# Kernel optimization log

Measured on AMD Instinct MI355X. Metric: run time of the kernel, lower is better.

Reference implementation:

```python
import jax, jax.numpy as jnp
import numpy as np

D_MODEL = 1024
NUM_HEADS = 16
D_K = D_MODEL // NUM_HEADS
BATCH = 4
SEQ = 2048


def setup_inputs() -> dict:
    key = jax.random.key(0)
    ks = jax.random.split(key, 12)
    s = 0.02
    inp = {
        "Q": jax.random.normal(ks[0], (BATCH, SEQ, D_MODEL), jnp.float32),
        "K": jax.random.normal(ks[1], (BATCH, SEQ, D_MODEL), jnp.float32),
        "V": jax.random.normal(ks[2], (BATCH, SEQ, D_MODEL), jnp.float32),
        "mask": jnp.tril(jnp.ones((SEQ, SEQ), jnp.int32)),  # causal: 0 = masked
        "Wq": jax.random.normal(ks[3], (D_MODEL, D_MODEL), jnp.float32) * s,
        "bq": jax.random.normal(ks[4], (D_MODEL,), jnp.float32) * s,
        "Wk": jax.random.normal(ks[5], (D_MODEL, D_MODEL), jnp.float32) * s,
        "bk": jax.random.normal(ks[6], (D_MODEL,), jnp.float32) * s,
        "Wv": jax.random.normal(ks[7], (D_MODEL, D_MODEL), jnp.float32) * s,
        "bv": jax.random.normal(ks[8], (D_MODEL,), jnp.float32) * s,
        "Wo": jax.random.normal(ks[9], (D_MODEL, D_MODEL), jnp.float32) * s,
        "bo": jax.random.normal(ks[10], (D_MODEL,), jnp.float32) * s,
    }
    return inp


def _split_heads(x):
    # (b, s, d_model) -> (b, h, s, d_k)
    b, s, _ = x.shape
    return x.reshape(b, s, NUM_HEADS, D_K).transpose(0, 2, 1, 3)


def reference(Q, K, V, mask, Wq, bq, Wk, bk, Wv, bv, Wo, bo):
    # Linear projections (torch Linear: x @ W^T + b)
    q = _split_heads(Q @ Wq.T + bq)  # (b, h, s, dk)
    k = _split_heads(K @ Wk.T + bk)
    v = _split_heads(V @ Wv.T + bv)
    scale = 1.0 / jnp.sqrt(jnp.asarray(D_K, q.dtype))
    scores = jnp.einsum("bhqd,bhkd->bhqk", q, k) * scale  # (b, h, s, s)
    scores = jnp.where(mask == 0, jnp.asarray(-jnp.inf, scores.dtype), scores)
    attn = jax.nn.softmax(scores, axis=-1)
    out = jnp.einsum("bhqk,bhkd->bhqd", attn, v)  # (b, h, s, dk)
    b, h, s, dk = out.shape
    out = out.transpose(0, 2, 1, 3).reshape(b, s, h * dk)  # combine heads
    return out @ Wo.T + bo
```

## Files before the change

kernel.cpp:

```cpp
#include <hip/hip_runtime.h>


typedef _Float16 f16;
typedef _Float16 f16x8 __attribute__((ext_vector_type(8)));
typedef _Float16 f16x4 __attribute__((ext_vector_type(4)));
typedef float floatx4 __attribute__((ext_vector_type(4)));

#define SEQ 2048
#define DM 1024
#define NH 16
#define DK 64
#define MR 8192

__device__ __forceinline__ void gl_lds16(const void* g, void* lds) {
    __builtin_amdgcn_global_load_lds(
        (const __attribute__((address_space(1))) unsigned int*)g,
        (__attribute__((address_space(3))) unsigned int*)lds,
        16, 0, 0);
}

struct ConvArgs {
    const float* s[7];
    f16* d[7];
};

__global__ __launch_bounds__(256) void convk(ConvArgs a) {
    int bx = blockIdx.x;
    int t, base;
    if (bx < 3 * 8192) { t = bx / 8192; base = bx - t * 8192; }
    else { int r = bx - 3 * 8192; t = 3 + r / 1024; base = r - (t - 3) * 1024; }
    int i = base * 256 + threadIdx.x;
    float4 v = ((const float4*)a.s[t])[i];
    f16x4 o;
    o.x = (f16)v.x; o.y = (f16)v.y; o.z = (f16)v.z; o.w = (f16)v.w;
    ((f16x4*)a.d[t])[i] = o;
}

template <int MODE>
__device__ __forceinline__ void gemm_body(
    const f16* __restrict__ A, const f16* __restrict__ W,
    const float* __restrict__ bias, void* __restrict__ outp,
    int m0, int n0, f16* As, f16* Bs)
{
    const int tid = threadIdx.x;
    const int wave = tid >> 6, lane = tid & 63;
    const int quad = lane >> 4, ln = lane & 15;
    const int wr = wave >> 1, wc = wave & 1;

    floatx4 acc[4][4] = {};

    for (int kt = 0; kt < 16; ++kt) {
        const int k0 = kt * 64;
#pragma unroll
        for (int s = 0; s < 4; ++s) {
            int c = s * 256 + tid;
            int row = c >> 3, lc = (c & 7) ^ (row & 7);
            gl_lds16(A + (size_t)(m0 + row) * 1024 + k0 + lc * 8,
                     (char*)As + (s * 256 + wave * 64) * 16);
        }
#pragma unroll
        for (int s = 0; s < 4; ++s) {
            int c = s * 256 + tid;
            int row = c >> 3, lc = (c & 7) ^ (row & 7);
            gl_lds16(W + (size_t)(n0 + row) * 1024 + k0 + lc * 8,
                     (char*)Bs + (s * 256 + wave * 64) * 16);
        }
        __syncthreads();
#pragma unroll
        for (int kk = 0; kk < 64; kk += 32) {
            const int cb = kk >> 3;
            f16x8 af[4], bf[4];
#pragma unroll
            for (int i = 0; i < 4; ++i) {
                int row = wr * 64 + i * 16 + ln;
                af[i] = *(const f16x8*)&As[row * 64 + (((cb + quad) ^ (ln & 7)) << 3)];
            }
#pragma unroll
            for (int j = 0; j < 4; ++j) {
                int row = wc * 64 + j * 16 + ln;
                bf[j] = *(const f16x8*)&Bs[row * 64 + (((cb + quad) ^ (ln & 7)) << 3)];
            }
#pragma unroll
            for (int i = 0; i < 4; ++i)
#pragma unroll
                for (int j = 0; j < 4; ++j)
                    acc[i][j] = __builtin_amdgcn_mfma_f32_16x16x32_f16(
                        af[i], bf[j], acc[i][j], 0, 0, 0);
        }
        __syncthreads();
    }

#pragma unroll
    for (int i = 0; i < 4; ++i) {
#pragma unroll
        for (int j = 0; j < 4; ++j) {
            int col = n0 + wc * 64 + j * 16 + ln;
            float bc = bias[col];
            int rowb = m0 + wr * 64 + i * 16 + quad * 4;
#pragma unroll
            for (int r = 0; r < 4; ++r) {
                float v = acc[i][j][r] + bc;
                int rm = rowb + r;
                if (MODE == 2) {
                    ((float*)outp)[(size_t)rm * 1024 + col] = v;
                } else {
                    int bb = rm >> 11, ss = rm & 2047;
                    int hh = col >> 6, dd = col & 63;
                    f16* o = (f16*)outp;
                    if (MODE == 0)
                        o[(((size_t)(bb * 16 + hh)) * 2048 + ss) * 64 + dd] = (f16)v;
                    else
                        o[(((size_t)(bb * 16 + hh)) * 64 + dd) * 2048 + ss] = (f16)v;
                }
            }
        }
    }
}

struct G3Args {
    const f16* A[3]; const f16* W[3]; const float* b[3]; f16* o[3];
};

__global__ __launch_bounds__(256, 4) void gemm_qkv(G3Args g) {
    __shared__ alignas(16) f16 As[128 * 64];
    __shared__ alignas(16) f16 Bs[128 * 64];
    const int z = blockIdx.z;
    const int m0 = blockIdx.x * 128, n0 = blockIdx.y * 128;
    if (z < 2)
        gemm_body<0>(g.A[z], g.W[z], g.b[z], g.o[z], m0, n0, As, Bs);
    else
        gemm_body<1>(g.A[2], g.W[2], g.b[2], g.o[2], m0, n0, As, Bs);
}

__global__ __launch_bounds__(256, 4) void gemm_out(
    const f16* __restrict__ A, const f16* __restrict__ W,
    const float* __restrict__ bias, float* __restrict__ outp)
{
    __shared__ alignas(16) f16 As[128 * 64];
    __shared__ alignas(16) f16 Bs[128 * 64];
    gemm_body<2>(A, W, bias, outp, blockIdx.x * 128, blockIdx.y * 128, As, Bs);
}

template <bool DIAG>
__device__ __forceinline__ void attn_iter(
    const f16* kb, const f16* vb, int k0, int q0,
    f16* ks, f16* vs, f16* pslot,
    int tid, int wave, int quad, int ln,
    const f16x8 (&aq)[2][2], const f16x8& ones,
    floatx4 (&oacc)[2][4], floatx4 (&lacc)[2])
{
#pragma unroll
    for (int s = 0; s < 4; ++s) {
        int c = s * 256 + tid;
        int row = c >> 3, lc = (c & 7) ^ (row & 7);
        gl_lds16(kb + (size_t)(k0 + row) * 64 + lc * 8,
                 (char*)ks + (s * 256 + wave * 64) * 16);
    }
#pragma unroll
    for (int s = 0; s < 4; ++s) {
        int c = s * 256 + tid;
        int row = c >> 4, lc = (c & 15) ^ (row & 15);
        gl_lds16(vb + (size_t)row * SEQ + k0 + lc * 8,
                 (char*)vs + (s * 256 + wave * 64) * 16);
    }
    __syncthreads();

    floatx4 sacc[2][8] = {};
#pragma unroll
    for (int kk = 0; kk < 2; ++kk) {
        const int pc = ((kk * 4 + quad) ^ (ln & 7)) << 3;
#pragma unroll
        for (int nt = 0; nt < 8; ++nt) {
            f16x8 bk = *(const f16x8*)&ks[(nt * 16 + ln) * 64 + pc];
#pragma unroll
            for (int mt = 0; mt < 2; ++mt)
                sacc[mt][nt] = __builtin_amdgcn_mfma_f32_16x16x32_f16(
                    aq[mt][kk], bk, sacc[mt][nt], 0, 0, 0);
        }
    }

#pragma unroll
    for (int mt = 0; mt < 2; ++mt) {
        const int rowb = q0 + wave * 32 + mt * 16 + quad * 4;
#pragma unroll
        for (int nt = 0; nt < 8; ++nt) {
            const int lch = nt * 2 + (ln >> 3);
            const int off = ln & 7;
            const int colv = k0 + nt * 16 + ln;
#pragma unroll
            for (int r = 0; r < 4; ++r) {
                float t = sacc[mt][nt][r];
                if (DIAG && colv > rowb + r) t = -1e30f;
                float p = __builtin_amdgcn_exp2f(t);
                const int rp = mt * 16 + quad * 4 + r;
                const int sw = (rp & 15) ^ (((rp >> 3) & 1) << 1);
                pslot[rp * 128 + ((lch ^ sw) << 3) + off] = (f16)p;
            }
        }
    }

#pragma unroll
    for (int kk4 = 0; kk4 < 4; ++kk4) {
        f16x8 ap[2];
#pragma unroll
        for (int mt = 0; mt < 2; ++mt) {
            const int rp = mt * 16 + ln;
            const int sw = (rp & 15) ^ (((rp >> 3) & 1) << 1);
            ap[mt] = *(const f16x8*)&pslot[rp * 128 + (((kk4 * 4 + quad) ^ sw) << 3)];
            lacc[mt] = __builtin_amdgcn_mfma_f32_16x16x32_f16(
                ap[mt], ones, lacc[mt], 0, 0, 0);
        }
#pragma unroll
        for (int nt2 = 0; nt2 < 4; ++nt2) {
            int row = nt2 * 16 + ln;
            f16x8 bv = *(const f16x8*)&vs[row * 128 + (((kk4 * 4 + quad) ^ ln) << 3)];
#pragma unroll
            for (int mt = 0; mt < 2; ++mt)
                oacc[mt][nt2] = __builtin_amdgcn_mfma_f32_16x16x32_f16(
                    ap[mt], bv, oacc[mt][nt2], 0, 0, 0);
        }
    }
    __syncthreads();
}

__global__ __launch_bounds__(256, 2) void attn_kernel(
    const f16* __restrict__ Qp, const f16* __restrict__ Kp,
    const f16* __restrict__ Vt, f16* __restrict__ Op)
{
    __shared__ alignas(16) f16 ks[128 * 64];
    __shared__ alignas(16) f16 vs[64 * 128];
    __shared__ alignas(16) f16 ps[128 * 128];

    const int tid = threadIdx.x;
    const int wave = tid >> 6, lane = tid & 63;
    const int quad = lane >> 4, ln = lane & 15;
    const int bh = blockIdx.x;
    const f16* qb = Qp + (size_t)bh * SEQ * DK;
    const f16* kb = Kp + (size_t)bh * SEQ * DK;
    const f16* vb = Vt + (size_t)bh * DK * SEQ;
    const int b = bh >> 4, h = bh & 15;

    f16* pslot = ps + wave * 4096;

    f16x8 ones;
#pragma unroll
    for (int e = 0; e < 8; ++e) ones[e] = (f16)1.0f;

    for (int half = 0; half < 2; ++half) {
        const int jt = half ? (15 - blockIdx.y) : blockIdx.y;
        const int q0 = jt * 128;

#pragma unroll
        for (int s = 0; s < 4; ++s) {
            int c = s * 256 + tid;
            int row = c >> 3, lc = (c & 7) ^ (row & 7);
            gl_lds16(qb + (size_t)(q0 + row) * 64 + lc * 8,
                     (char*)ps + (s * 256 + wave * 64) * 16);
        }
        __syncthreads();
        f16x8 aq[2][2];
#pragma unroll
        for (int mt = 0; mt < 2; ++mt)
#pragma unroll
            for (int kk = 0; kk < 2; ++kk) {
                int row = wave * 32 + mt * 16 + ln;
                f16x8 v = *(const f16x8*)&ps[row * 64 + (((kk * 4 + quad) ^ (ln & 7)) << 3)];
#pragma unroll
                for (int e = 0; e < 8; ++e)
                    v[e] = v[e] * (f16)0.18033688f;
                aq[mt][kk] = v;
            }

        floatx4 oacc[2][4] = {};
        floatx4 lacc[2] = {};

        const int nk = jt + 1;
        for (int kt = 0; kt < nk - 1; ++kt)
            attn_iter<false>(kb, vb, kt * 128, q0, ks, vs, pslot,
                             tid, wave, quad, ln, aq, ones, oacc, lacc);
        attn_iter<true>(kb, vb, (nk - 1) * 128, q0, ks, vs, pslot,
                        tid, wave, quad, ln, aq, ones, oacc, lacc);

#pragma unroll
        for (int mt = 0; mt < 2; ++mt) {
            int rowb = q0 + wave * 32 + mt * 16 + quad * 4;
            float inv[4];
#pragma unroll
            for (int r = 0; r < 4; ++r) inv[r] = 1.0f / lacc[mt][r];
#pragma unroll
            for (int nt2 = 0; nt2 < 4; ++nt2) {
                int col = h * 64 + nt2 * 16 + ln;
#pragma unroll
                for (int r = 0; r < 4; ++r) {
                    float v = oacc[mt][nt2][r] * inv[r];
                    Op[((size_t)b * SEQ + rowb + r) * DM + col] = (f16)v;
                }
            }
        }
    }
}

extern "C" void kernel_launch(void* const* d_in, const int* in_sizes, int n_in,
                              void* d_out, int out_size, void* d_ws, size_t ws_size,
                              hipStream_t stream) {
    const float* Q  = (const float*)d_in[0];
    const float* K  = (const float*)d_in[1];
    const float* V  = (const float*)d_in[2];
    const float* Wq = (const float*)d_in[4];
    const float* bq = (const float*)d_in[5];
    const float* Wk = (const float*)d_in[6];
    const float* bk = (const float*)d_in[7];
    const float* Wv = (const float*)d_in[8];
    const float* bv = (const float*)d_in[9];
    const float* Wo = (const float*)d_in[10];
    const float* bo = (const float*)d_in[11];

    char* ws = (char*)d_ws;
    f16* Xq  = (f16*)(ws);
    f16* Xk  = Xq + (size_t)MR * DM;
    f16* Xv  = Xk + (size_t)MR * DM;
    f16* Wqb = Xv + (size_t)MR * DM;
    f16* Wkb = Wqb + (size_t)DM * DM;
    f16* Wvb = Wkb + (size_t)DM * DM;
    f16* Wob = Wvb + (size_t)DM * DM;
    f16* qp  = Wob + (size_t)DM * DM;
    f16* kp  = qp + (size_t)MR * DM;
    f16* vtp = kp + (size_t)MR * DM;

    ConvArgs ca;
    ca.s[0] = Q;  ca.d[0] = Xq;
    ca.s[1] = K;  ca.d[1] = Xk;
    ca.s[2] = V;  ca.d[2] = Xv;
    ca.s[3] = Wq; ca.d[3] = Wqb;
    ca.s[4] = Wk; ca.d[4] = Wkb;
    ca.s[5] = Wv; ca.d[5] = Wvb;
    ca.s[6] = Wo; ca.d[6] = Wob;
    convk<<<3 * 8192 + 4 * 1024, 256, 0, stream>>>(ca);

    G3Args g;
    g.A[0] = Xq; g.W[0] = Wqb; g.b[0] = bq; g.o[0] = qp;
    g.A[1] = Xk; g.W[1] = Wkb; g.b[1] = bk; g.o[1] = kp;
    g.A[2] = Xv; g.W[2] = Wvb; g.b[2] = bv; g.o[2] = vtp;
    gemm_qkv<<<dim3(64, 8, 3), 256, 0, stream>>>(g);

    attn_kernel<<<dim3(64, 8), 256, 0, stream>>>(qp, kp, vtp, Xq);

    gemm_out<<<dim3(64, 8), 256, 0, stream>>>(Xq, Wob, bo, (float*)d_out);
}
```

Measured before the change: 314.3 us.

## Fuse fp32-to-fp16 activation conversion into QKV projection GEMM loads

Result: no change. 311.7 us (-0.9%).

```diff
diff --git a/kernel.cpp b/kernel.cpp
--- a/kernel.cpp
+++ b/kernel.cpp
@@ -4,6 +4,7 @@
 typedef _Float16 f16;
 typedef _Float16 f16x8 __attribute__((ext_vector_type(8)));
 typedef _Float16 f16x4 __attribute__((ext_vector_type(4)));
+typedef __fp16 h16x2 __attribute__((ext_vector_type(2)));
 typedef float floatx4 __attribute__((ext_vector_type(4)));
 
 #define SEQ 2048
@@ -19,16 +20,24 @@
         16, 0, 0);
 }
 
+__device__ __forceinline__ f16x8 cvt8(const float4& a, const float4& b) {
+    h16x2 h0 = __builtin_amdgcn_cvt_pkrtz(a.x, a.y);
+    h16x2 h1 = __builtin_amdgcn_cvt_pkrtz(a.z, a.w);
+    h16x2 h2 = __builtin_amdgcn_cvt_pkrtz(b.x, b.y);
+    h16x2 h3 = __builtin_amdgcn_cvt_pkrtz(b.z, b.w);
+    f16x8 o;
+    o[0] = (f16)h0[0]; o[1] = (f16)h0[1]; o[2] = (f16)h1[0]; o[3] = (f16)h1[1];
+    o[4] = (f16)h2[0]; o[5] = (f16)h2[1]; o[6] = (f16)h3[0]; o[7] = (f16)h3[1];
+    return o;
+}
+
 struct ConvArgs {
-    const float* s[7];
-    f16* d[7];
+    const float* s[4];
+    f16* d[4];
 };
 
-__global__ __launch_bounds__(256) void convk(ConvArgs a) {
-    int bx = blockIdx.x;
-    int t, base;
-    if (bx < 3 * 8192) { t = bx / 8192; base = bx - t * 8192; }
-    else { int r = bx - 3 * 8192; t = 3 + r / 1024; base = r - (t - 3) * 1024; }
+__global__ __launch_bounds__(256) void convw(ConvArgs a) {
+    int t = blockIdx.x >> 10, base = blockIdx.x & 1023;
     int i = base * 256 + threadIdx.x;
     float4 v = ((const float4*)a.s[t])[i];
     f16x4 o;
@@ -36,9 +45,9 @@
     ((f16x4*)a.d[t])[i] = o;
 }
 
-template <int MODE>
+template <int MODE, bool AFUSE>
 __device__ __forceinline__ void gemm_body(
-    const f16* __restrict__ A, const f16* __restrict__ W,
+    const void* __restrict__ A, const f16* __restrict__ W,
     const float* __restrict__ bias, void* __restrict__ outp,
     int m0, int n0, f16* As, f16* Bs)
 {
@@ -55,15 +64,31 @@
         for (int s = 0; s < 4; ++s) {
             int c = s * 256 + tid;
             int row = c >> 3, lc = (c & 7) ^ (row & 7);
-            gl_lds16(A + (size_t)(m0 + row) * 1024 + k0 + lc * 8,
-                     (char*)As + (s * 256 + wave * 64) * 16);
-        }
-#pragma unroll
-        for (int s = 0; s < 4; ++s) {
-            int c = s * 256 + tid;
-            int row = c >> 3, lc = (c & 7) ^ (row & 7);
             gl_lds16(W + (size_t)(n0 + row) * 1024 + k0 + lc * 8,
                      (char*)Bs + (s * 256 + wave * 64) * 16);
+        }
+        if constexpr (AFUSE) {
+            const float* Af = (const float*)A;
+            float4 u[4], v[4];
+#pragma unroll
+            for (int s = 0; s < 4; ++s) {
+                int c = s * 256 + tid;
+                int row = c >> 3, lc = (c & 7) ^ (row & 7);
+                const float* src = Af + (size_t)(m0 + row) * 1024 + k0 + lc * 8;
+                u[s] = ((const float4*)src)[0];
+                v[s] = ((const float4*)src)[1];
+            }
+#pragma unroll
+            for (int s = 0; s < 4; ++s)
+                ((f16x8*)As)[s * 256 + tid] = cvt8(u[s], v[s]);
+        } else {
+#pragma unroll
+            for (int s = 0; s < 4; ++s) {
+                int c = s * 256 + tid;
+                int row = c >> 3, lc = (c & 7) ^ (row & 7);
+                gl_lds16((const f16*)A + (size_t)(m0 + row) * 1024 + k0 + lc * 8,
+                         (char*)As + (s * 256 + wave * 64) * 16);
+            }
         }
         __syncthreads();
 #pragma unroll
@@ -118,27 +143,28 @@
 }
 
 struct G3Args {
-    const f16* A[3]; const f16* W[3]; const float* b[3]; f16* o[3];
+    const float* A[3]; const f16* W[3]; const float* b[3]; f16* o[3];
 };
 
-__global__ __launch_bounds__(256, 4) void gemm_qkv(G3Args g) {
+__global__ __launch_bounds__(256, 2) void gemm_qkv(G3Args g) {
     __shared__ alignas(16) f16 As[128 * 64];
     __shared__ alignas(16) f16 Bs[128 * 64];
     const int z = blockIdx.z;
     const int m0 = blockIdx.x * 128, n0 = blockIdx.y * 128;
     if (z < 2)
-        gemm_body<0>(g.A[z], g.W[z], g.b[z], g.o[z], m0, n0, As, Bs);
+        gemm_body<0, true>(g.A[z], g.W[z], g.b[z], g.o[z], m0, n0, As, Bs);
     else
-        gemm_body<1>(g.A[2], g.W[2], g.b[2], g.o[2], m0, n0, As, Bs);
-}
-
-__global__ __launch_bounds__(256, 4) void gemm_out(
+        gemm_body<1, true>(g.A[2], g.W[2], g.b[2], g.o[2], m0, n0, As, Bs);
+}
+
+__global__ __launch_bounds__(256, 2) void gemm_out(
     const f16* __restrict__ A, const f16* __restrict__ W,
     const float* __restrict__ bias, float* __restrict__ outp)
 {
     __shared__ alignas(16) f16 As[128 * 64];
     __shared__ alignas(16) f16 Bs[128 * 64];
-    gemm_body<2>(A, W, bias, outp, blockIdx.x * 128, blockIdx.y * 128, As, Bs);
+    gemm_body<2, false>(A, W, bias, outp, blockIdx.x * 128, blockIdx.y * 128,
+                        As, Bs);
 }
 
 template <bool DIAG>
@@ -316,34 +342,29 @@
     const float* bo = (const float*)d_in[11];
 
     char* ws = (char*)d_ws;
-    f16* Xq  = (f16*)(ws);
-    f16* Xk  = Xq + (size_t)MR * DM;
-    f16* Xv  = Xk + (size_t)MR * DM;
-    f16* Wqb = Xv + (size_t)MR * DM;
+    f16* Wqb = (f16*)ws;
     f16* Wkb = Wqb + (size_t)DM * DM;
     f16* Wvb = Wkb + (size_t)DM * DM;
     f16* Wob = Wvb + (size_t)DM * DM;
     f16* qp  = Wob + (size_t)DM * DM;
     f16* kp  = qp + (size_t)MR * DM;
     f16* vtp = kp + (size_t)MR * DM;
+    f16* ao  = vtp + (size_t)MR * DM;
 
     ConvArgs ca;
-    ca.s[0] = Q;  ca.d[0] = Xq;
-    ca.s[1] = K;  ca.d[1] = Xk;
-    ca.s[2] = V;  ca.d[2] = Xv;
-    ca.s[3] = Wq; ca.d[3] = Wqb;
-    ca.s[4] = Wk; ca.d[4] = Wkb;
-    ca.s[5] = Wv; ca.d[5] = Wvb;
-    ca.s[6] = Wo; ca.d[6] = Wob;
-    convk<<<3 * 8192 + 4 * 1024, 256, 0, stream>>>(ca);
+    ca.s[0] = Wq; ca.d[0] = Wqb;
+    ca.s[1] = Wk; ca.d[1] = Wkb;
+    ca.s[2] = Wv; ca.d[2] = Wvb;
+    ca.s[3] = Wo; ca.d[3] = Wob;
+    convw<<<4 * 1024, 256, 0, stream>>>(ca);
 
     G3Args g;
-    g.A[0] = Xq; g.W[0] = Wqb; g.b[0] = bq; g.o[0] = qp;
-    g.A[1] = Xk; g.W[1] = Wkb; g.b[1] = bk; g.o[1] = kp;
-    g.A[2] = Xv; g.W[2] = Wvb; g.b[2] = bv; g.o[2] = vtp;
+    g.A[0] = Q; g.W[0] = Wqb; g.b[0] = bq; g.o[0] = qp;
+    g.A[1] = K; g.W[1] = Wkb; g.b[1] = bk; g.o[1] = kp;
+    g.A[2] = V; g.W[2] = Wvb; g.b[2] = bv; g.o[2] = vtp;
     gemm_qkv<<<dim3(64, 8, 3), 256, 0, stream>>>(g);
 
-    attn_kernel<<<dim3(64, 8), 256, 0, stream>>>(qp, kp, vtp, Xq);
-
-    gemm_out<<<dim3(64, 8), 256, 0, stream>>>(Xq, Wob, bo, (float*)d_out);
-}
+    attn_kernel<<<dim3(64, 8), 256, 0, stream>>>(qp, kp, vtp, ao);
+
+    gemm_out<<<dim3(64, 8), 256, 0, stream>>>(ao, Wob, bo, (float*)d_out);
+}
```
